# Performance work log

Measured on AMD Instinct MI355X. Metric: run time of the kernel, lower is better.

## Reference

```python
import jax, jax.numpy as jnp
import numpy as np

MODEL_DIM = 2048
RANK = 128
N_HEADS = 16
B, S = 4, 2048


def setup_inputs() -> dict:
    key = jax.random.key(0)
    k_x, k_q, k_k, k_v, k_o = jax.random.split(key, 5)
    X = jax.random.normal(k_x, (B, S, MODEL_DIM), dtype=jnp.float32)
    mask = jnp.ones((B, S, S), dtype=bool)
    W_Q = jax.random.normal(k_q, (MODEL_DIM, RANK * N_HEADS), dtype=jnp.float32)
    W_K = jax.random.normal(k_k, (MODEL_DIM, RANK * N_HEADS), dtype=jnp.float32)
    W_V = jax.random.normal(k_v, (MODEL_DIM, RANK * N_HEADS), dtype=jnp.float32)
    W_O = jax.random.normal(k_o, (RANK * N_HEADS, RANK), dtype=jnp.float32)
    return {"X": X, "mask": mask, "W_Q": W_Q, "W_K": W_K, "W_V": W_V, "W_O": W_O}


def reference(X, mask, W_Q, W_K, W_V, W_O):
    b, s, _ = X.shape
    scale = 1.0 / (RANK ** 0.5)
    # project and split heads: (b, s, h*r) -> (b, h, s, r)
    def split_heads(Y):
        return Y.reshape(b, s, N_HEADS, RANK).transpose(0, 2, 1, 3)
    Q = split_heads(X @ W_Q)
    K = split_heads(X @ W_K)
    V = split_heads(X @ W_V)
    scores = jnp.einsum('bhir,bhjr->bhij', Q, K) * scale
    scores = jnp.where(mask[:, None, :, :], scores, -jnp.inf)
    probs = jax.nn.softmax(scores, axis=-1)
    attn = jnp.einsum('bhij,bhjr->bhir', probs, V)
    attn = attn.transpose(0, 2, 1, 3).reshape(b, s, N_HEADS * RANK)
    return attn @ W_O
```

## Files before the change

### kernel.cpp

```cpp
#include <hip/hip_runtime.h>
#include <cstdint>
#include <math.h>

typedef short bf16x8 __attribute__((ext_vector_type(8)));
typedef float f32x4 __attribute__((ext_vector_type(4)));

__device__ __forceinline__ unsigned short f2bf(float x) {
  union { float f; uint32_t u; } v; v.f = x;
  return (unsigned short)((v.u + 0x7FFFu + ((v.u >> 16) & 1u)) >> 16);
}
__device__ __forceinline__ float bf2f(unsigned short h) {
  union { uint32_t u; float f; } v; v.u = ((uint32_t)h) << 16;
  return v.f;
}

__device__ __forceinline__ void ld_lds16(const unsigned short* g, unsigned short* l) {
  auto gp = (const __attribute__((address_space(1))) unsigned short*)(uintptr_t)g;
  auto lp = (__attribute__((address_space(3))) unsigned short*)(uint32_t)(uintptr_t)l;
  __builtin_amdgcn_global_load_lds(gp, lp, 16, 0, 0);
}

#define DMA_COL(lane) ((((lane) & 3) ^ (((lane) >> 3) & 3)) * 8)
#define SWZ(l15) ((((l15) >> 1) & 3) * 8)
#define DMA_COL64(lane) ((((lane) & 7) ^ (((lane) >> 3) & 7)) * 8)

__global__ __launch_bounds__(256) void split_f32(const float* __restrict__ src,
                                                 unsigned short* __restrict__ hi,
                                                 unsigned short* __restrict__ lo, int n) {
  int i = (blockIdx.x * 256 + threadIdx.x) * 4;
  if (i >= n) return;
  float4 v = *(const float4*)(src + i);
  ushort4 h, l;
  h.x = f2bf(v.x); l.x = f2bf(v.x - bf2f(h.x));
  h.y = f2bf(v.y); l.y = f2bf(v.y - bf2f(h.y));
  h.z = f2bf(v.z); l.z = f2bf(v.z - bf2f(h.z));
  h.w = f2bf(v.w); l.w = f2bf(v.w - bf2f(h.w));
  *(ushort4*)(hi + i) = h;
  *(ushort4*)(lo + i) = l;
}

template<bool LO>
__global__ __launch_bounds__(256) void tsplit(const float* __restrict__ W,
                                              unsigned short* __restrict__ hiT,
                                              unsigned short* __restrict__ loT,
                                              int K, int N) {
  __shared__ float tile[32][33];
  const int tx = threadIdx.x, ty = threadIdx.y;
  const int bx = blockIdx.x, by = blockIdx.y;
#pragma unroll
  for (int i = 0; i < 4; ++i)
    tile[ty + i * 8][tx] = W[(size_t)(by * 32 + ty + i * 8) * N + bx * 32 + tx];
  __syncthreads();
#pragma unroll
  for (int i = 0; i < 4; ++i) {
    float v = tile[tx][ty + i * 8];
    size_t o = (size_t)(bx * 32 + ty + i * 8) * K + by * 32 + tx;
    unsigned short h = f2bf(v);
    hiT[o] = h;
    if (LO) loT[o] = f2bf(v - bf2f(h));
  }
}

__global__ __launch_bounds__(512, 2) void gemm_qkv3(
    const unsigned short* __restrict__ Xhi, const unsigned short* __restrict__ Xlo,
    const unsigned short* __restrict__ Wq_h, const unsigned short* __restrict__ Wq_l,
    const unsigned short* __restrict__ Wk_h, const unsigned short* __restrict__ Wk_l,
    const unsigned short* __restrict__ Wv_h,
    unsigned short* __restrict__ Qhi, unsigned short* __restrict__ Qlo,
    unsigned short* __restrict__ Khi, unsigned short* __restrict__ Klo,
    unsigned short* __restrict__ Vt, float qscale) {
  __shared__ unsigned short sm[65536];
  const int K = 2048, N = 2048;
  const int gx = gridDim.x, gy = gridDim.y;
  const int perz = (gx * gy) >> 3;
  const int lid = blockIdx.x + gx * (blockIdx.y + gy * blockIdx.z);
  const int xcd = lid & 7, idx = lid >> 3;
  const int z = idx / perz;
  const int wiz = xcd * perz + (idx - z * perz);
  const int bx = wiz % gx;
  const int by = wiz / gx;
  const int t = threadIdx.x;
  const int wave = t >> 6, lane = t & 63, quad = lane >> 4, l15 = lane & 15;
  const int m0 = by * 256, n0 = bx * 128;
  const int wm = (wave >> 1) * 64, wn = (wave & 1) * 64;

  if (z == 0) {
    const int cq0 = (quad * 8) ^ SWZ(l15);
    const unsigned short* gch[8];
    int loff[8];
#pragma unroll
    for (int j = 0; j < 8; ++j) {
      const int c = wave * 8 + j;
      const unsigned short* base; int row0, toff, rg;
      if (c < 16)      { base = Xhi;  row0 = m0; toff = 0;     rg = c; }
      else if (c < 32) { base = Xlo;  row0 = m0; toff = 8192;  rg = c - 16; }
      else if (c < 40) { base = Wq_h; row0 = n0; toff = 16384; rg = c - 32; }
      else if (c < 48) { base = Wq_l; row0 = n0; toff = 20480; rg = c - 40; }
      else if (c < 56) { base = Wk_h; row0 = n0; toff = 24576; rg = c - 48; }
      else             { base = Wk_l; row0 = n0; toff = 28672; rg = c - 56; }
      gch[j] = base + (size_t)(row0 + rg * 16 + (lane >> 2)) * K + DMA_COL(lane);
      loff[j] = toff + rg * 512;
    }
    auto stage = [&](int buf, int k0) {
#pragma unroll
      for (int j = 0; j < 8; ++j)
        ld_lds16(gch[j] + k0, sm + buf * 32768 + loff[j]);
    };
    f32x4 aq[4][4] = {}, ak[4][4] = {};
    stage(0, 0);
    asm volatile("s_waitcnt vmcnt(0)" ::: "memory");
    __builtin_amdgcn_s_barrier();
    __builtin_amdgcn_sched_barrier(0);
    int cur = 0;
    for (int tix = 0; tix < 64; ++tix) {
      if (tix + 1 < 64) stage(cur ^ 1, (tix + 1) * 32);
      const unsigned short* bufp = sm + cur * 32768;
      bf16x8 ah[4], al[4], bh[4], bl[4];
#pragma unroll
      for (int mb = 0; mb < 4; ++mb) {
        ah[mb] = *(const bf16x8*)&bufp[(wm + mb * 16 + l15) * 32 + cq0];
        al[mb] = *(const bf16x8*)&bufp[8192 + (wm + mb * 16 + l15) * 32 + cq0];
      }
#pragma unroll
      for (int nb = 0; nb < 4; ++nb) {
        bh[nb] = *(const bf16x8*)&bufp[16384 + (wn + nb * 16 + l15) * 32 + cq0];
        bl[nb] = *(const bf16x8*)&bufp[20480 + (wn + nb * 16 + l15) * 32 + cq0];
      }
      __builtin_amdgcn_s_setprio(1);
#pragma unroll
      for (int mb = 0; mb < 4; ++mb)
#pragma unroll
        for (int nb = 0; nb < 4; ++nb) {
          aq[mb][nb] = __builtin_amdgcn_mfma_f32_16x16x32_bf16(ah[mb], bh[nb], aq[mb][nb], 0, 0, 0);
          aq[mb][nb] = __builtin_amdgcn_mfma_f32_16x16x32_bf16(ah[mb], bl[nb], aq[mb][nb], 0, 0, 0);
          aq[mb][nb] = __builtin_amdgcn_mfma_f32_16x16x32_bf16(al[mb], bh[nb], aq[mb][nb], 0, 0, 0);
        }
      __builtin_amdgcn_s_setprio(0);
      __builtin_amdgcn_sched_barrier(0);
#pragma unroll
      for (int nb = 0; nb < 4; ++nb) {
        bh[nb] = *(const bf16x8*)&bufp[24576 + (wn + nb * 16 + l15) * 32 + cq0];
        bl[nb] = *(const bf16x8*)&bufp[28672 + (wn + nb * 16 + l15) * 32 + cq0];
      }
      __builtin_amdgcn_s_setprio(1);
#pragma unroll
      for (int mb = 0; mb < 4; ++mb)
#pragma unroll
        for (int nb = 0; nb < 4; ++nb) {
          ak[mb][nb] = __builtin_amdgcn_mfma_f32_16x16x32_bf16(ah[mb], bh[nb], ak[mb][nb], 0, 0, 0);
          ak[mb][nb] = __builtin_amdgcn_mfma_f32_16x16x32_bf16(ah[mb], bl[nb], ak[mb][nb], 0, 0, 0);
          ak[mb][nb] = __builtin_amdgcn_mfma_f32_16x16x32_bf16(al[mb], bh[nb], ak[mb][nb], 0, 0, 0);
        }
      __builtin_amdgcn_s_setprio(0);
      if (tix + 1 < 64) {
        asm volatile("s_waitcnt vmcnt(0)" ::: "memory");
        __builtin_amdgcn_s_barrier();
        __builtin_amdgcn_sched_barrier(0);
      }
      cur ^= 1;
    }
#pragma unroll
    for (int mb = 0; mb < 4; ++mb)
#pragma unroll
      for (int nb = 0; nb < 4; ++nb)
#pragma unroll
        for (int r = 0; r < 4; ++r) {
          int row = m0 + wm + mb * 16 + quad * 4 + r;
          int col = n0 + wn + nb * 16 + l15;
          float vq = aq[mb][nb][r] * qscale;
          unsigned short hq = f2bf(vq);
          Qhi[(size_t)row * N + col] = hq;
          Qlo[(size_t)row * N + col] = f2bf(vq - bf2f(hq));
          float vk = ak[mb][nb][r];
          unsigned short hk = f2bf(vk);
          Khi[(size_t)row * N + col] = hk;
          Klo[(size_t)row * N + col] = f2bf(vk - bf2f(hk));
        }
  } else {
    const unsigned short* gch[6];
    int loff[6];
#pragma unroll
    for (int j = 0; j < 6; ++j) {
      const int c = wave * 6 + j;
      const unsigned short* base; int row0, toff, rg;
      if (c < 32) { base = Xhi;  row0 = m0; toff = 0;     rg = c; }
      else        { base = Wv_h; row0 = n0; toff = 16384; rg = c - 32; }
      gch[j] = base + (size_t)(row0 + rg * 8 + (lane >> 3)) * K + DMA_COL64(lane);
      loff[j] = toff + rg * 512;
    }
    auto stage = [&](int buf, int k0) {
#pragma unroll
      for (int j = 0; j < 6; ++j)
        ld_lds16(gch[j] + k0, sm + buf * 24576 + loff[j]);
    };
    f32x4 acc[4][4] = {};
    stage(0, 0);
    asm volatile("s_waitcnt vmcnt(0)" ::: "memory");
    __builtin_amdgcn_s_barrier();
    __builtin_amdgcn_sched_barrier(0);
    int cur = 0;
    for (int tix = 0; tix < 32; ++tix) {
      if (tix + 1 < 32) stage(cur ^ 1, (tix + 1) * 64);
      const unsigned short* bufp = sm + cur * 24576;
      bf16x8 a[2][4], b[2][4];
#pragma unroll
      for (int kk = 0; kk < 2; ++kk) {
#pragma unroll
        for (int mb = 0; mb < 4; ++mb) {
          const int row = wm + mb * 16 + l15;
          a[kk][mb] = *(const bf16x8*)&bufp[row * 64 + (((kk * 4 + quad) ^ (row & 7)) * 8)];
        }
#pragma unroll
        for (int nb = 0; nb < 4; ++nb) {
          const int row = wn + nb * 16 + l15;
          b[kk][nb] = *(const bf16x8*)&bufp[16384 + row * 64 + (((kk * 4 + quad) ^ (row & 7)) * 8)];
        }
      }
      __builtin_amdgcn_s_setprio(1);
#pragma unroll
      for (int kk = 0; kk < 2; ++kk)
#pragma unroll
        for (int mb = 0; mb < 4; ++mb)
#pragma unroll
          for (int nb = 0; nb < 4; ++nb)
            acc[mb][nb] = __builtin_amdgcn_mfma_f32_16x16x32_bf16(a[kk][mb], b[kk][nb], acc[mb][nb], 0, 0, 0);
      __builtin_amdgcn_s_setprio(0);
      if (tix + 1 < 32) {
        asm volatile("s_waitcnt vmcnt(0)" ::: "memory");
        __builtin_amdgcn_s_barrier();
        __builtin_amdgcn_sched_barrier(0);
      }
      cur ^= 1;
    }
    __syncthreads();
#pragma unroll
    for (int mb = 0; mb < 4; ++mb)
#pragma unroll
      for (int nb = 0; nb < 4; ++nb) {
        ushort4 pk;
        pk.x = f2bf(acc[mb][nb][0]);
        pk.y = f2bf(acc[mb][nb][1]);
        pk.z = f2bf(acc[mb][nb][2]);
        pk.w = f2bf(acc[mb][nb][3]);
        *(ushort4*)&sm[(wn + nb * 16 + l15) * 264 + wm + mb * 16 + quad * 4] = pk;
      }
    __syncthreads();
    const int bb = m0 >> 11;
    const int mloc = m0 & 2047;
    unsigned short* Vb = Vt + (size_t)bb * 2048 * 2048;
#pragma unroll
    for (int jj = 0; jj < 8; ++jj) {
      int idx2 = jj * 512 + t;
      int n = idx2 >> 5, mu = idx2 & 31;
      uint4 v = *(uint4*)&sm[n * 264 + mu * 8];
      *(uint4*)(Vb + (size_t)(n0 + n) * 2048 + mloc + mu * 8) = v;
    }
  }
}

__global__ __launch_bounds__(256) void gemm_out(
    const unsigned short* __restrict__ Ahi, const unsigned short* __restrict__ Bhi,
    float* __restrict__ out, int M, int N, int K, int ldk) {
  __shared__ unsigned short sm[3 * 8192];
  const int z = blockIdx.z;
  const int t = threadIdx.x;
  const int wave = t >> 6, lane = t & 63, quad = lane >> 4, l15 = lane & 15;
  const int wm = (wave & 1) * 64, wn = (wave >> 1) * 64;
  const int m0 = blockIdx.y * 128, n0 = blockIdx.x * 128;
  const int cq0 = (quad * 8) ^ SWZ(l15);
  const unsigned short* gsrc = (wave < 2) ? Ahi : Bhi;
  const int boff = (wave < 2) ? 0 : 4096;
  const int row0 = (wave < 2) ? m0 : n0;
  const int jb = (wave & 1) * 4;
  const unsigned short* gbase = gsrc + (size_t)(row0 + (lane >> 2)) * K
                                + (size_t)z * ldk + DMA_COL(lane);
  const int nst = ldk / 32;
  auto stage = [&](int buf, int ks) {
#pragma unroll
    for (int j = 0; j < 4; ++j)
      ld_lds16(gbase + (size_t)((jb + j) * 16) * K + ks * 32,
               sm + buf * 8192 + boff + (jb + j) * 512);
  };
  f32x4 acc[4][4] = {};
  stage(0, 0);
  stage(1, 1);
  asm volatile("s_waitcnt vmcnt(4)" ::: "memory");
  __builtin_amdgcn_s_barrier();
  __builtin_amdgcn_sched_barrier(0);
  int cur = 0, st = 2;
  for (int tix = 0; tix < nst; ++tix) {
    if (tix + 2 < nst) stage(st, tix + 2);
    const unsigned short* bufp = sm + cur * 8192;
    bf16x8 ah[4], bh[4];
#pragma unroll
    for (int mb = 0; mb < 4; ++mb)
      ah[mb] = *(const bf16x8*)&bufp[(wm + mb * 16 + l15) * 32 + cq0];
#pragma unroll
    for (int nb = 0; nb < 4; ++nb)
      bh[nb] = *(const bf16x8*)&bufp[4096 + (wn + nb * 16 + l15) * 32 + cq0];
    __builtin_amdgcn_s_setprio(1);
#pragma unroll
    for (int mb = 0; mb < 4; ++mb)
#pragma unroll
      for (int nb = 0; nb < 4; ++nb)
        acc[mb][nb] = __builtin_amdgcn_mfma_f32_16x16x32_bf16(ah[mb], bh[nb], acc[mb][nb], 0, 0, 0);
    __builtin_amdgcn_s_setprio(0);
    if (tix + 2 < nst) asm volatile("s_waitcnt vmcnt(4)" ::: "memory");
    else               asm volatile("s_waitcnt vmcnt(0)" ::: "memory");
    __builtin_amdgcn_s_barrier();
    __builtin_amdgcn_sched_barrier(0);
    cur = cur == 2 ? 0 : cur + 1;
    st = st == 2 ? 0 : st + 1;
  }
  float* of = out + (size_t)z * M * N;
#pragma unroll
  for (int mb = 0; mb < 4; ++mb)
#pragma unroll
    for (int nb = 0; nb < 4; ++nb)
#pragma unroll
      for (int r = 0; r < 4; ++r) {
        int row = m0 + wm + mb * 16 + quad * 4 + r;
        int col = n0 + wn + nb * 16 + l15;
        of[(size_t)row * N + col] = acc[mb][nb][r];
      }
}

__global__ __launch_bounds__(256) void reduceN(const float* __restrict__ p,
                                               float* __restrict__ out, int n, int nsl) {
  int i = (blockIdx.x * 256 + threadIdx.x) * 4;
  if (i >= n) return;
  float4 acc = *(const float4*)(p + i);
  for (int s = 1; s < nsl; ++s) {
    float4 v = *(const float4*)(p + (size_t)s * n + i);
    acc.x += v.x; acc.y += v.y; acc.z += v.z; acc.w += v.w;
  }
  *(float4*)(out + i) = acc;
}

__global__ __launch_bounds__(256, 2) void attn_mfma(
    const unsigned short* __restrict__ Qhi, const unsigned short* __restrict__ Qlo,
    const unsigned short* __restrict__ Khi, const unsigned short* __restrict__ Klo,
    const unsigned short* __restrict__ Vt, unsigned short* __restrict__ Ob, int S) {
  __shared__ unsigned short Kh_s[3 * 4096];
  __shared__ unsigned short Kl_s[3 * 4096];
  __shared__ unsigned short V_s[3 * 4096];
  __shared__ unsigned short P_s[4 * 640];
  const int t = threadIdx.x;
  const int wave = t >> 6, lane = t & 63, quad = lane >> 4, l15 = lane & 15;
  const int bidall = blockIdx.x;
  const size_t boff = (size_t)(bidall >> 8) * (2048 * 2048);
  Qhi += boff; Qlo += boff; Khi += boff; Klo += boff; Vt += boff; Ob += boff;
  const int bid = bidall & 255;
  const int xcd = bid & 7, slot = bid >> 3;
  const int head = (xcd << 1) | (slot >> 4);
  const int qblk = slot & 15;
  const size_t hoff = (size_t)head * 128;
  const int cq0 = (quad * 8) ^ SWZ(l15);

  bf16x8 qh[2][4], ql[2][4];
#pragma unroll
  for (int g = 0; g < 2; ++g) {
    const int qb = qblk * 128 + g * 64 + wave * 16;
#pragma unroll
    for (int kb = 0; kb < 4; ++kb) {
      size_t off = (size_t)(qb + l15) * 2048 + hoff + kb * 32 + quad * 8;
      qh[g][kb] = *(const bf16x8*)(Qhi + off);
      ql[g][kb] = *(const bf16x8*)(Qlo + off);
    }
  }
  f32x4 o[2][8] = {};
  float m_run[2] = {-INFINITY, -INFINITY}, l_run[2] = {0.f, 0.f};

  const int lr = lane >> 2, lc = DMA_COL(lane);
  const unsigned short* gKh = Khi + (size_t)lr * 2048 + hoff + wave * 32 + lc;
  const unsigned short* gKl = Klo + (size_t)lr * 2048 + hoff + wave * 32 + lc;
  const unsigned short* gV  = Vt + (hoff + wave * 32 + lr) * (size_t)S + lc;
  unsigned short* Pw = P_s + wave * 640;

  auto stage = [&](int buf, int kpos) {
    const int b4 = buf * 4096 + wave * 1024;
#pragma unroll
    for (int i = 0; i < 2; ++i) {
      ld_lds16(gKh + (size_t)(kpos + i * 16) * 2048, Kh_s + b4 + i * 512);
      ld_lds16(gKl + (size_t)(kpos + i * 16) * 2048, Kl_s + b4 + i * 512);
      ld_lds16(gV + (size_t)(i * 16) * S + kpos,      V_s + b4 + i * 512);
    }
  };
  stage(0, 0);
  stage(1, 32);
  asm volatile("s_waitcnt vmcnt(6)" ::: "memory");
  __builtin_amdgcn_s_barrier();
  __builtin_amdgcn_sched_barrier(0);

  int cur = 0, st = 2;
  for (int tix = 0; tix < 64; ++tix) {
    if (tix + 2 < 64) stage(st, (tix + 2) * 32);
    const int cb = cur * 4096;
    f32x4 s[2][2] = {};
    __builtin_amdgcn_s_setprio(1);
#pragma unroll
    for (int mb = 0; mb < 2; ++mb)
#pragma unroll
      for (int kb = 0; kb < 4; ++kb) {
        bf16x8 kh = *(bf16x8*)&Kh_s[cb + kb * 1024 + (mb * 16 + l15) * 32 + cq0];
        bf16x8 kl = *(bf16x8*)&Kl_s[cb + kb * 1024 + (mb * 16 + l15) * 32 + cq0];
        s[0][mb] = __builtin_amdgcn_mfma_f32_16x16x32_bf16(kh, qh[0][kb], s[0][mb], 0, 0, 0);
        s[0][mb] = __builtin_amdgcn_mfma_f32_16x16x32_bf16(kh, ql[0][kb], s[0][mb], 0, 0, 0);
        s[0][mb] = __builtin_amdgcn_mfma_f32_16x16x32_bf16(kl, qh[0][kb], s[0][mb], 0, 0, 0);
        s[1][mb] = __builtin_amdgcn_mfma_f32_16x16x32_bf16(kh, qh[1][kb], s[1][mb], 0, 0, 0);
        s[1][mb] = __builtin_amdgcn_mfma_f32_16x16x32_bf16(kh, ql[1][kb], s[1][mb], 0, 0, 0);
        s[1][mb] = __builtin_amdgcn_mfma_f32_16x16x32_bf16(kl, qh[1][kb], s[1][mb], 0, 0, 0);
      }
    __builtin_amdgcn_s_setprio(0);

    bf16x8 pf[2];
#pragma unroll
    for (int g = 0; g < 2; ++g) {
      float mt = s[g][0][0];
#pragma unroll
      for (int r = 1; r < 4; ++r) mt = fmaxf(mt, s[g][0][r]);
#pragma unroll
      for (int r = 0; r < 4; ++r) mt = fmaxf(mt, s[g][1][r]);
      mt = fmaxf(mt, __shfl_xor(mt, 16));
      mt = fmaxf(mt, __shfl_xor(mt, 32));
      if (!__all(mt <= m_run[g] + 8.f)) {
        const float m_new = fmaxf(m_run[g], mt);
        const float alpha = __builtin_amdgcn_exp2f(m_run[g] - m_new);
        l_run[g] *= alpha;
#pragma unroll
        for (int rb = 0; rb < 8; ++rb)
#pragma unroll
          for (int r = 0; r < 4; ++r) o[g][rb][r] *= alpha;
        m_run[g] = m_new;
      }
      float p[8];
#pragma unroll
      for (int mb = 0; mb < 2; ++mb)
#pragma unroll
        for (int r = 0; r < 4; ++r)
          p[mb * 4 + r] = __builtin_amdgcn_exp2f(s[g][mb][r] - m_run[g]);
      float rs = p[0];
#pragma unroll
      for (int j = 1; j < 8; ++j) rs += p[j];
      rs += __shfl_xor(rs, 16);
      rs += __shfl_xor(rs, 32);
      l_run[g] += rs;
#pragma unroll
      for (int mb = 0; mb < 2; ++mb) {
        ushort4 pk;
        pk.x = f2bf(p[mb * 4 + 0]);
        pk.y = f2bf(p[mb * 4 + 1]);
        pk.z = f2bf(p[mb * 4 + 2]);
        pk.w = f2bf(p[mb * 4 + 3]);
        *(ushort4*)&Pw[l15 * 40 + mb * 16 + quad * 4] = pk;
      }
      pf[g] = *(bf16x8*)&Pw[l15 * 40 + quad * 8];
    }
    __builtin_amdgcn_s_setprio(1);
#pragma unroll
    for (int rb = 0; rb < 8; ++rb) {
      bf16x8 vb = *(bf16x8*)&V_s[cb + (rb * 16 + l15) * 32 + cq0];
      o[0][rb] = __builtin_amdgcn_mfma_f32_16x16x32_bf16(vb, pf[0], o[0][rb], 0, 0, 0);
      o[1][rb] = __builtin_amdgcn_mfma_f32_16x16x32_bf16(vb, pf[1], o[1][rb], 0, 0, 0);
    }
    __builtin_amdgcn_s_setprio(0);
    if (tix + 2 < 64) asm volatile("s_waitcnt vmcnt(6)" ::: "memory");
    else              asm volatile("s_waitcnt vmcnt(0)" ::: "memory");
    __builtin_amdgcn_s_barrier();
    __builtin_amdgcn_sched_barrier(0);
    cur = cur == 2 ? 0 : cur + 1;
    st = st == 2 ? 0 : st + 1;
  }
#pragma unroll
  for (int g = 0; g < 2; ++g) {
    const int qb = qblk * 128 + g * 64 + wave * 16;
    const float inv = 1.0f / l_run[g];
#pragma unroll
    for (int rb = 0; rb < 8; ++rb) {
      ushort4 pk;
      pk.x = f2bf(o[g][rb][0] * inv);
      pk.y = f2bf(o[g][rb][1] * inv);
      pk.z = f2bf(o[g][rb][2] * inv);
      pk.w = f2bf(o[g][rb][3] * inv);
      *(ushort4*)(Ob + (size_t)(qb + l15) * 2048 + hoff + rb * 16 + quad * 4) = pk;
    }
  }
}

extern "C" void kernel_launch(void* const* d_in, const int* in_sizes, int n_in,
                              void* d_out, int out_size, void* d_ws, size_t ws_size,
                              hipStream_t stream) {
  (void)in_sizes; (void)n_in; (void)out_size;
  const float* X   = (const float*)d_in[0];
  const float* W_Q = (const float*)d_in[2];
  const float* W_K = (const float*)d_in[3];
  const float* W_V = (const float*)d_in[4];
  const float* W_O = (const float*)d_in[5];
  float* out = (float*)d_out;

  const int S = 2048, HD = 2048;
  const size_t P = (size_t)HD * HD;
  unsigned short* w = (unsigned short*)d_ws;
  unsigned short* WqThi = w;
  unsigned short* WqTlo = w + P;
  unsigned short* WkThi = w + 2 * P;
  unsigned short* WkTlo = w + 3 * P;
  unsigned short* WvThi = w + 4 * P;
  unsigned short* WoThi = w + 5 * P;
  unsigned short* base6 = w + 5 * P + P / 16;

  const float qscale = 0.12752551286084109f;

  dim3 bT(32, 8);
  tsplit<true ><<<dim3(64, 64), bT, 0, stream>>>(W_Q, WqThi, WqTlo, HD, HD);
  tsplit<true ><<<dim3(64, 64), bT, 0, stream>>>(W_K, WkThi, WkTlo, HD, HD);
  tsplit<false><<<dim3(64, 64), bT, 0, stream>>>(W_V, WvThi, nullptr, HD, HD);
  tsplit<false><<<dim3(4, 64),  bT, 0, stream>>>(W_O, WoThi, nullptr, HD, 128);

  const size_t elW = 5 * P + P / 16;
  const size_t need2 = (elW + 14 * P) * 2;
  const size_t need1 = (elW + 7 * P) * 2;
  int C; bool tight = false;
  if (ws_size >= need2)      C = 2;
  else if (ws_size >= need1) C = 1;
  else { C = 1; tight = true; }

  const size_t CP = (size_t)C * P;
  unsigned short* Xhi = base6;
  unsigned short* Xlo = base6 + CP;
  unsigned short* Qhi = base6 + 2 * CP;
  unsigned short* Qlo = base6 + 3 * CP;
  unsigned short* Khi = base6 + 4 * CP;
  unsigned short* Klo = base6 + 5 * CP;
  unsigned short* Vt  = tight ? Xlo : base6 + 6 * CP;
  unsigned short* attnB = Xhi;
  float* fpart = (float*)Qhi;

  const int M = C * S;
  const int zn = 16 / C;
  const int ldk = HD / zn;
  const int NOUT = M * 128;

  for (int c = 0; c < 4 / C; ++c) {
    split_f32<<<C * 4096, 256, 0, stream>>>(X + (size_t)c * CP, Xhi, Xlo, (int)CP);
    gemm_qkv3<<<dim3(16, C * 8, 2), 512, 0, stream>>>(
        Xhi, Xlo, WqThi, WqTlo, WkThi, WkTlo, WvThi,
        Qhi, Qlo, Khi, Klo, Vt, qscale);
    attn_mfma<<<C * 256, 256, 0, stream>>>(Qhi, Qlo, Khi, Klo, Vt, attnB, S);
    gemm_out<<<dim3(1, C * 16, zn), 256, 0, stream>>>(attnB, WoThi, fpart, M, 128, HD, ldk);
    reduceN<<<NOUT / 1024, 256, 0, stream>>>(fpart, out + (size_t)c * NOUT, NOUT, zn);
  }
}
```

Measured before the change: 870.2 us.

## Split fused QKV GEMM into separate QK and V kernels; merge weight transposes

The single gemm_qkv3 kernel, which used a z-index to run either the heavy 3-pass Q/K path or the lighter V path, is split into two kernels. gemm_qk uses 512 threads with 256x128 tiles, and gemm_v uses 256 threads with 128x128 tiles and smaller LDS, so each can be sized and scheduled for its own workload. This is meant to remove the imbalance of heterogeneous blocks sharing one grid and the LDS over-allocation on the V path. The four weight transpose/split launches are also merged into one launch with a z dimension. The cost is an extra kernel launch per chunk, and the V GEMM no longer overlaps with the QK GEMM within a single grid.

```diff
diff --git a/kernel.cpp b/kernel.cpp
--- a/kernel.cpp
+++ b/kernel.cpp
@@ -39,12 +39,20 @@
   *(ushort4*)(lo + i) = l;
 }
 
-template<bool LO>
-__global__ __launch_bounds__(256) void tsplit(const float* __restrict__ W,
-                                              unsigned short* __restrict__ hiT,
-                                              unsigned short* __restrict__ loT,
-                                              int K, int N) {
+__global__ __launch_bounds__(256) void tsplit4(
+    const float* __restrict__ Wq, const float* __restrict__ Wk,
+    const float* __restrict__ Wv, const float* __restrict__ Wo,
+    unsigned short* __restrict__ qh, unsigned short* __restrict__ ql,
+    unsigned short* __restrict__ kh, unsigned short* __restrict__ kl,
+    unsigned short* __restrict__ vh, unsigned short* __restrict__ oh) {
   __shared__ float tile[32][33];
+  const int z = blockIdx.z;
+  if (z == 3 && blockIdx.x >= 4) return;
+  const float* W = z == 0 ? Wq : z == 1 ? Wk : z == 2 ? Wv : Wo;
+  unsigned short* hiT = z == 0 ? qh : z == 1 ? kh : z == 2 ? vh : oh;
+  unsigned short* loT = z == 1 ? kl : ql;
+  const bool LO = z < 2;
+  const int K = 2048, N = (z == 3) ? 128 : 2048;
   const int tx = threadIdx.x, ty = threadIdx.y;
   const int bx = blockIdx.x, by = blockIdx.y;
 #pragma unroll
@@ -61,200 +69,209 @@
   }
 }
 
-__global__ __launch_bounds__(512, 2) void gemm_qkv3(
+__global__ __launch_bounds__(512, 2) void gemm_qk(
     const unsigned short* __restrict__ Xhi, const unsigned short* __restrict__ Xlo,
     const unsigned short* __restrict__ Wq_h, const unsigned short* __restrict__ Wq_l,
     const unsigned short* __restrict__ Wk_h, const unsigned short* __restrict__ Wk_l,
-    const unsigned short* __restrict__ Wv_h,
     unsigned short* __restrict__ Qhi, unsigned short* __restrict__ Qlo,
-    unsigned short* __restrict__ Khi, unsigned short* __restrict__ Klo,
-    unsigned short* __restrict__ Vt, float qscale) {
+    unsigned short* __restrict__ Khi, unsigned short* __restrict__ Klo, float qscale) {
   __shared__ unsigned short sm[65536];
   const int K = 2048, N = 2048;
   const int gx = gridDim.x, gy = gridDim.y;
-  const int perz = (gx * gy) >> 3;
-  const int lid = blockIdx.x + gx * (blockIdx.y + gy * blockIdx.z);
-  const int xcd = lid & 7, idx = lid >> 3;
-  const int z = idx / perz;
-  const int wiz = xcd * perz + (idx - z * perz);
+  const int lid = blockIdx.x + gx * blockIdx.y;
+  const int wiz = (lid & 7) * ((gx * gy) >> 3) + (lid >> 3);
   const int bx = wiz % gx;
   const int by = wiz / gx;
   const int t = threadIdx.x;
   const int wave = t >> 6, lane = t & 63, quad = lane >> 4, l15 = lane & 15;
   const int m0 = by * 256, n0 = bx * 128;
   const int wm = (wave >> 1) * 64, wn = (wave & 1) * 64;
-
-  if (z == 0) {
-    const int cq0 = (quad * 8) ^ SWZ(l15);
-    const unsigned short* gch[8];
-    int loff[8];
-#pragma unroll
-    for (int j = 0; j < 8; ++j) {
-      const int c = wave * 8 + j;
-      const unsigned short* base; int row0, toff, rg;
-      if (c < 16)      { base = Xhi;  row0 = m0; toff = 0;     rg = c; }
-      else if (c < 32) { base = Xlo;  row0 = m0; toff = 8192;  rg = c - 16; }
-      else if (c < 40) { base = Wq_h; row0 = n0; toff = 16384; rg = c - 32; }
-      else if (c < 48) { base = Wq_l; row0 = n0; toff = 20480; rg = c - 40; }
-      else if (c < 56) { base = Wk_h; row0 = n0; toff = 24576; rg = c - 48; }
-      else             { base = Wk_l; row0 = n0; toff = 28672; rg = c - 56; }
-      gch[j] = base + (size_t)(row0 + rg * 16 + (lane >> 2)) * K + DMA_COL(lane);
-      loff[j] = toff + rg * 512;
-    }
-    auto stage = [&](int buf, int k0) {
-#pragma unroll
-      for (int j = 0; j < 8; ++j)
-        ld_lds16(gch[j] + k0, sm + buf * 32768 + loff[j]);
-    };
-    f32x4 aq[4][4] = {}, ak[4][4] = {};
-    stage(0, 0);
-    asm volatile("s_waitcnt vmcnt(0)" ::: "memory");
-    __builtin_amdgcn_s_barrier();
+  const int cq0 = (quad * 8) ^ SWZ(l15);
+
+  const unsigned short* gch[8];
+  int loff[8];
+#pragma unroll
+  for (int j = 0; j < 8; ++j) {
+    const int c = wave * 8 + j;
+    const unsigned short* base; int row0, toff, rg;
+    if (c < 16)      { base = Xhi;  row0 = m0; toff = 0;     rg = c; }
+    else if (c < 32) { base = Xlo;  row0 = m0; toff = 8192;  rg = c - 16; }
+    else if (c < 40) { base = Wq_h; row0 = n0; toff = 16384; rg = c - 32; }
+    else if (c < 48) { base = Wq_l; row0 = n0; toff = 20480; rg = c - 40; }
+    else if (c < 56) { base = Wk_h; row0 = n0; toff = 24576; rg = c - 48; }
+    else             { base = Wk_l; row0 = n0; toff = 28672; rg = c - 56; }
+    gch[j] = base + (size_t)(row0 + rg * 16 + (lane >> 2)) * K + DMA_COL(lane);
+    loff[j] = toff + rg * 512;
+  }
+  auto stage = [&](int buf, int k0) {
+#pragma unroll
+    for (int j = 0; j < 8; ++j)
+      ld_lds16(gch[j] + k0, sm + buf * 32768 + loff[j]);
+  };
+  f32x4 aq[4][4] = {}, ak[4][4] = {};
+  stage(0, 0);
+  asm volatile("s_waitcnt vmcnt(0)" ::: "memory");
+  __builtin_amdgcn_s_barrier();
+  __builtin_amdgcn_sched_barrier(0);
+  int cur = 0;
+  for (int tix = 0; tix < 64; ++tix) {
+    if (tix + 1 < 64) stage(cur ^ 1, (tix + 1) * 32);
+    const unsigned short* bufp = sm + cur * 32768;
+    bf16x8 ah[4], al[4], bh[4], bl[4];
+#pragma unroll
+    for (int mb = 0; mb < 4; ++mb) {
+      ah[mb] = *(const bf16x8*)&bufp[(wm + mb * 16 + l15) * 32 + cq0];
+      al[mb] = *(const bf16x8*)&bufp[8192 + (wm + mb * 16 + l15) * 32 + cq0];
+    }
+#pragma unroll
+    for (int nb = 0; nb < 4; ++nb) {
+      bh[nb] = *(const bf16x8*)&bufp[16384 + (wn + nb * 16 + l15) * 32 + cq0];
+      bl[nb] = *(const bf16x8*)&bufp[20480 + (wn + nb * 16 + l15) * 32 + cq0];
+    }
+    __builtin_amdgcn_s_setprio(1);
+#pragma unroll
+    for (int mb = 0; mb < 4; ++mb)
+#pragma unroll
+      for (int nb = 0; nb < 4; ++nb) {
+        aq[mb][nb] = __builtin_amdgcn_mfma_f32_16x16x32_bf16(ah[mb], bh[nb], aq[mb][nb], 0, 0, 0);
+        aq[mb][nb] = __builtin_amdgcn_mfma_f32_16x16x32_bf16(ah[mb], bl[nb], aq[mb][nb], 0, 0, 0);
+        aq[mb][nb] = __builtin_amdgcn_mfma_f32_16x16x32_bf16(al[mb], bh[nb], aq[mb][nb], 0, 0, 0);
+      }
+    __builtin_amdgcn_s_setprio(0);
     __builtin_amdgcn_sched_barrier(0);
-    int cur = 0;
-    for (int tix = 0; tix < 64; ++tix) {
-      if (tix + 1 < 64) stage(cur ^ 1, (tix + 1) * 32);
-      const unsigned short* bufp = sm + cur * 32768;
-      bf16x8 ah[4], al[4], bh[4], bl[4];
+#pragma unroll
+    for (int nb = 0; nb < 4; ++nb) {
+      bh[nb] = *(const bf16x8*)&bufp[24576 + (wn + nb * 16 + l15) * 32 + cq0];
+      bl[nb] = *(const bf16x8*)&bufp[28672 + (wn + nb * 16 + l15) * 32 + cq0];
+    }
+    __builtin_amdgcn_s_setprio(1);
+#pragma unroll
+    for (int mb = 0; mb < 4; ++mb)
+#pragma unroll
+      for (int nb = 0; nb < 4; ++nb) {
+        ak[mb][nb] = __builtin_amdgcn_mfma_f32_16x16x32_bf16(ah[mb], bh[nb], ak[mb][nb], 0, 0, 0);
+        ak[mb][nb] = __builtin_amdgcn_mfma_f32_16x16x32_bf16(ah[mb], bl[nb], ak[mb][nb], 0, 0, 0);
+        ak[mb][nb] = __builtin_amdgcn_mfma_f32_16x16x32_bf16(al[mb], bh[nb], ak[mb][nb], 0, 0, 0);
+      }
+    __builtin_amdgcn_s_setprio(0);
+    if (tix + 1 < 64) {
+      asm volatile("s_waitcnt vmcnt(0)" ::: "memory");
+      __builtin_amdgcn_s_barrier();
+      __builtin_amdgcn_sched_barrier(0);
+    }
+    cur ^= 1;
+  }
+#pragma unroll
+  for (int mb = 0; mb < 4; ++mb)
+#pragma unroll
+    for (int nb = 0; nb < 4; ++nb)
+#pragma unroll
+      for (int r = 0; r < 4; ++r) {
+        int row = m0 + wm + mb * 16 + quad * 4 + r;
+        int col = n0 + wn + nb * 16 + l15;
+        float vq = aq[mb][nb][r] * qscale;
+        unsigned short hq = f2bf(vq);
+        Qhi[(size_t)row * N + col] = hq;
+        Qlo[(size_t)row * N + col] = f2bf(vq - bf2f(hq));
+        float vk = ak[mb][nb][r];
+        unsigned short hk = f2bf(vk);
+        Khi[(size_t)row * N + col] = hk;
+        Klo[(size_t)row * N + col] = f2bf(vk - bf2f(hk));
+      }
+}
+
+__global__ __launch_bounds__(256, 2) void gemm_v(
+    const unsigned short* __restrict__ Xhi, const unsigned short* __restrict__ Wv_h,
+    unsigned short* __restrict__ Vt) {
+  __shared__ unsigned short sm[32768];
+  const int K = 2048;
+  const int gx = gridDim.x, gy = gridDim.y;
+  const int lid = blockIdx.x + gx * blockIdx.y;
+  const int wiz = (lid & 7) * ((gx * gy) >> 3) + (lid >> 3);
+  const int bx = wiz % gx;
+  const int by = wiz / gx;
+  const int t = threadIdx.x;
+  const int wave = t >> 6, lane = t & 63, quad = lane >> 4, l15 = lane & 15;
+  const int m0 = by * 128, n0 = bx * 128;
+  const int wm = (wave >> 1) * 64, wn = (wave & 1) * 64;
+
+  const unsigned short* gch[8];
+  int loff[8];
+#pragma unroll
+  for (int j = 0; j < 8; ++j) {
+    const int c = wave * 8 + j;
+    const unsigned short* base; int row0, toff, rg;
+    if (c < 16) { base = Xhi;  row0 = m0; toff = 0;    rg = c; }
+    else        { base = Wv_h; row0 = n0; toff = 8192; rg = c - 16; }
+    gch[j] = base + (size_t)(row0 + rg * 8 + (lane >> 3)) * K + DMA_COL64(lane);
+    loff[j] = toff + rg * 512;
+  }
+  auto stage = [&](int buf, int k0) {
+#pragma unroll
+    for (int j = 0; j < 8; ++j)
+      ld_lds16(gch[j] + k0, sm + buf * 16384 + loff[j]);
+  };
+  f32x4 acc[4][4] = {};
+  stage(0, 0);
+  asm volatile("s_waitcnt vmcnt(0)" ::: "memory");
+  __builtin_amdgcn_s_barrier();
+  __builtin_amdgcn_sched_barrier(0);
+  int cur = 0;
+  for (int tix = 0; tix < 32; ++tix) {
+    if (tix + 1 < 32) stage(cur ^ 1, (tix + 1) * 64);
+    const unsigned short* bufp = sm + cur * 16384;
+    bf16x8 a[2][4], b[2][4];
+#pragma unroll
+    for (int kk = 0; kk < 2; ++kk) {
 #pragma unroll
       for (int mb = 0; mb < 4; ++mb) {
-        ah[mb] = *(const bf16x8*)&bufp[(wm + mb * 16 + l15) * 32 + cq0];
-        al[mb] = *(const bf16x8*)&bufp[8192 + (wm + mb * 16 + l15) * 32 + cq0];
+        const int row = wm + mb * 16 + l15;
+        a[kk][mb] = *(const bf16x8*)&bufp[row * 64 + (((kk * 4 + quad) ^ (row & 7)) * 8)];
       }
 #pragma unroll
       for (int nb = 0; nb < 4; ++nb) {
-        bh[nb] = *(const bf16x8*)&bufp[16384 + (wn + nb * 16 + l15) * 32 + cq0];
-        bl[nb] = *(const bf16x8*)&bufp[20480 + (wn + nb * 16 + l15) * 32 + cq0];
-      }
-      __builtin_amdgcn_s_setprio(1);
+        const int row = wn + nb * 16 + l15;
+        b[kk][nb] = *(const bf16x8*)&bufp[8192 + row * 64 + (((kk * 4 + quad) ^ (row & 7)) * 8)];
+      }
+    }
+    __builtin_amdgcn_s_setprio(1);
+#pragma unroll
+    for (int kk = 0; kk < 2; ++kk)
 #pragma unroll
       for (int mb = 0; mb < 4; ++mb)
 #pragma unroll
-        for (int nb = 0; nb < 4; ++nb) {
-          aq[mb][nb] = __builtin_amdgcn_mfma_f32_16x16x32_bf16(ah[mb], bh[nb], aq[mb][nb], 0, 0, 0);
-          aq[mb][nb] = __builtin_amdgcn_mfma_f32_16x16x32_bf16(ah[mb], bl[nb], aq[mb][nb], 0, 0, 0);
-          aq[mb][nb] = __builtin_amdgcn_mfma_f32_16x16x32_bf16(al[mb], bh[nb], aq[mb][nb], 0, 0, 0);
-        }
-      __builtin_amdgcn_s_setprio(0);
+        for (int nb = 0; nb < 4; ++nb)
+          acc[mb][nb] = __builtin_amdgcn_mfma_f32_16x16x32_bf16(a[kk][mb], b[kk][nb], acc[mb][nb], 0, 0, 0);
+    __builtin_amdgcn_s_setprio(0);
+    if (tix + 1 < 32) {
+      asm volatile("s_waitcnt vmcnt(0)" ::: "memory");
+      __builtin_amdgcn_s_barrier();
       __builtin_amdgcn_sched_barrier(0);
-#pragma unroll
-      for (int nb = 0; nb < 4; ++nb) {
-        bh[nb] = *(const bf16x8*)&bufp[24576 + (wn + nb * 16 + l15) * 32 + cq0];
-        bl[nb] = *(const bf16x8*)&bufp[28672 + (wn + nb * 16 + l15) * 32 + cq0];
-      }
-      __builtin_amdgcn_s_setprio(1);
-#pragma unroll
-      for (int mb = 0; mb < 4; ++mb)
-#pragma unroll
-        for (int nb = 0; nb < 4; ++nb) {
-          ak[mb][nb] = __builtin_amdgcn_mfma_f32_16x16x32_bf16(ah[mb], bh[nb], ak[mb][nb], 0, 0, 0);
-          ak[mb][nb] = __builtin_amdgcn_mfma_f32_16x16x32_bf16(ah[mb], bl[nb], ak[mb][nb], 0, 0, 0);
-          ak[mb][nb] = __builtin_amdgcn_mfma_f32_16x16x32_bf16(al[mb], bh[nb], ak[mb][nb], 0, 0, 0);
-        }
-      __builtin_amdgcn_s_setprio(0);
-      if (tix + 1 < 64) {
-        asm volatile("s_waitcnt vmcnt(0)" ::: "memory");
-        __builtin_amdgcn_s_barrier();
-        __builtin_amdgcn_sched_barrier(0);
-      }
-      cur ^= 1;
-    }
-#pragma unroll
-    for (int mb = 0; mb < 4; ++mb)
-#pragma unroll
-      for (int nb = 0; nb < 4; ++nb)
-#pragma unroll
-        for (int r = 0; r < 4; ++r) {
-          int row = m0 + wm + mb * 16 + quad * 4 + r;
-          int col = n0 + wn + nb * 16 + l15;
-          float vq = aq[mb][nb][r] * qscale;
-          unsigned short hq = f2bf(vq);
-          Qhi[(size_t)row * N + col] = hq;
-          Qlo[(size_t)row * N + col] = f2bf(vq - bf2f(hq));
-          float vk = ak[mb][nb][r];
-          unsigned short hk = f2bf(vk);
-          Khi[(size_t)row * N + col] = hk;
-          Klo[(size_t)row * N + col] = f2bf(vk - bf2f(hk));
-        }
-  } else {
-    const unsigned short* gch[6];
-    int loff[6];
-#pragma unroll
-    for (int j = 0; j < 6; ++j) {
-      const int c = wave * 6 + j;
-      const unsigned short* base; int row0, toff, rg;
-      if (c < 32) { base = Xhi;  row0 = m0; toff = 0;     rg = c; }
-      else        { base = Wv_h; row0 = n0; toff = 16384; rg = c - 32; }
-      gch[j] = base + (size_t)(row0 + rg * 8 + (lane >> 3)) * K + DMA_COL64(lane);
-      loff[j] = toff + rg * 512;
-    }
-    auto stage = [&](int buf, int k0) {
-#pragma unroll
-      for (int j = 0; j < 6; ++j)
-        ld_lds16(gch[j] + k0, sm + buf * 24576 + loff[j]);
-    };
-    f32x4 acc[4][4] = {};
-    stage(0, 0);
-    asm volatile("s_waitcnt vmcnt(0)" ::: "memory");
-    __builtin_amdgcn_s_barrier();
-    __builtin_amdgcn_sched_barrier(0);
-    int cur = 0;
-    for (int tix = 0; tix < 32; ++tix) {
-      if (tix + 1 < 32) stage(cur ^ 1, (tix + 1) * 64);
-      const unsigned short* bufp = sm + cur * 24576;
-      bf16x8 a[2][4], b[2][4];
-#pragma unroll
-      for (int kk = 0; kk < 2; ++kk) {
-#pragma unroll
-        for (int mb = 0; mb < 4; ++mb) {
-          const int row = wm + mb * 16 + l15;
-          a[kk][mb] = *(const bf16x8*)&bufp[row * 64 + (((kk * 4 + quad) ^ (row & 7)) * 8)];
-        }
-#pragma unroll
-        for (int nb = 0; nb < 4; ++nb) {
-          const int row = wn + nb * 16 + l15;
-          b[kk][nb] = *(const bf16x8*)&bufp[16384 + row * 64 + (((kk * 4 + quad) ^ (row & 7)) * 8)];
-        }
-      }
-      __builtin_amdgcn_s_setprio(1);
-#pragma unroll
-      for (int kk = 0; kk < 2; ++kk)
-#pragma unroll
-        for (int mb = 0; mb < 4; ++mb)
-#pragma unroll
-          for (int nb = 0; nb < 4; ++nb)
-            acc[mb][nb] = __builtin_amdgcn_mfma_f32_16x16x32_bf16(a[kk][mb], b[kk][nb], acc[mb][nb], 0, 0, 0);
-      __builtin_amdgcn_s_setprio(0);
-      if (tix + 1 < 32) {
-        asm volatile("s_waitcnt vmcnt(0)" ::: "memory");
-        __builtin_amdgcn_s_barrier();
-        __builtin_amdgcn_sched_barrier(0);
-      }
-      cur ^= 1;
-    }
-    __syncthreads();
-#pragma unroll
-    for (int mb = 0; mb < 4; ++mb)
-#pragma unroll
-      for (int nb = 0; nb < 4; ++nb) {
-        ushort4 pk;
-        pk.x = f2bf(acc[mb][nb][0]);
-        pk.y = f2bf(acc[mb][nb][1]);
-        pk.z = f2bf(acc[mb][nb][2]);
-        pk.w = f2bf(acc[mb][nb][3]);
-        *(ushort4*)&sm[(wn + nb * 16 + l15) * 264 + wm + mb * 16 + quad * 4] = pk;
-      }
-    __syncthreads();
-    const int bb = m0 >> 11;
-    const int mloc = m0 & 2047;
-    unsigned short* Vb = Vt + (size_t)bb * 2048 * 2048;
-#pragma unroll
-    for (int jj = 0; jj < 8; ++jj) {
-      int idx2 = jj * 512 + t;
-      int n = idx2 >> 5, mu = idx2 & 31;
-      uint4 v = *(uint4*)&sm[n * 264 + mu * 8];
-      *(uint4*)(Vb + (size_t)(n0 + n) * 2048 + mloc + mu * 8) = v;
-    }
+    }
+    cur ^= 1;
+  }
+  __syncthreads();
+#pragma unroll
+  for (int mb = 0; mb < 4; ++mb)
+#pragma unroll
+    for (int nb = 0; nb < 4; ++nb) {
+      ushort4 pk;
+      pk.x = f2bf(acc[mb][nb][0]);
+      pk.y = f2bf(acc[mb][nb][1]);
+      pk.z = f2bf(acc[mb][nb][2]);
+      pk.w = f2bf(acc[mb][nb][3]);
+      *(ushort4*)&sm[(wn + nb * 16 + l15) * 136 + wm + mb * 16 + quad * 4] = pk;
+    }
+  __syncthreads();
+  const int bb = m0 >> 11;
+  const int mloc = m0 & 2047;
+  unsigned short* Vb = Vt + (size_t)bb * 2048 * 2048;
+#pragma unroll
+  for (int jj = 0; jj < 8; ++jj) {
+    int idx = jj * 256 + t;
+    int n = idx >> 4, mu = idx & 15;
+    uint4 v = *(uint4*)&sm[n * 136 + mu * 8];
+    *(uint4*)(Vb + (size_t)(n0 + n) * 2048 + mloc + mu * 8) = v;
   }
 }
 
@@ -511,11 +528,8 @@
 
   const float qscale = 0.12752551286084109f;
 
-  dim3 bT(32, 8);
-  tsplit<true ><<<dim3(64, 64), bT, 0, stream>>>(W_Q, WqThi, WqTlo, HD, HD);
-  tsplit<true ><<<dim3(64, 64), bT, 0, stream>>>(W_K, WkThi, WkTlo, HD, HD);
-  tsplit<false><<<dim3(64, 64), bT, 0, stream>>>(W_V, WvThi, nullptr, HD, HD);
-  tsplit<false><<<dim3(4, 64),  bT, 0, stream>>>(W_O, WoThi, nullptr, HD, 128);
+  tsplit4<<<dim3(64, 64, 4), dim3(32, 8), 0, stream>>>(
+      W_Q, W_K, W_V, W_O, WqThi, WqTlo, WkThi, WkTlo, WvThi, WoThi);
 
   const size_t elW = 5 * P + P / 16;
   const size_t need2 = (elW + 14 * P) * 2;
@@ -543,9 +557,9 @@
 
   for (int c = 0; c < 4 / C; ++c) {
     split_f32<<<C * 4096, 256, 0, stream>>>(X + (size_t)c * CP, Xhi, Xlo, (int)CP);
-    gemm_qkv3<<<dim3(16, C * 8, 2), 512, 0, stream>>>(
-        Xhi, Xlo, WqThi, WqTlo, WkThi, WkTlo, WvThi,
-        Qhi, Qlo, Khi, Klo, Vt, qscale);
+    gemm_qk<<<dim3(16, C * 8), 512, 0, stream>>>(
+        Xhi, Xlo, WqThi, WqTlo, WkThi, WkTlo, Qhi, Qlo, Khi, Klo, qscale);
+    gemm_v<<<dim3(16, C * 16), 256, 0, stream>>>(Xhi, WvThi, Vt);
     attn_mfma<<<C * 256, 256, 0, stream>>>(Qhi, Qlo, Khi, Klo, Vt, attnB, S);
     gemm_out<<<dim3(1, C * 16, zn), 256, 0, stream>>>(attnB, WoThi, fpart, M, 128, HD, ldk);
     reduceN<<<NOUT / 1024, 256, 0, stream>>>(fpart, out + (size_t)c * NOUT, NOUT, zn);
```

Result: slower. 924.3 us (+6.2%).
